# Performance work log

Hardware: AMD Instinct MI355X
Metric: run time of the kernel (lower is better)

Reference implementation:

```python
import jax, jax.numpy as jnp
import numpy as np
from math import sqrt

DIM = 1024
RANK = 64
B, T = 4, 4096

def _xavier(key, shape):
    fan_in, fan_out = shape[1], shape[0]
    limit = sqrt(6.0 / (fan_in + fan_out))
    return jax.random.uniform(key, shape, jnp.float32, -limit, limit)

def setup_inputs() -> dict:
    key = jax.random.key(0)
    kx, kq, kk, kv = jax.random.split(key, 4)
    return {
        "x": jax.random.normal(kx, (B, T, DIM), jnp.float32),
        "Q": _xavier(kq, (RANK, DIM)),
        "K": _xavier(kk, (RANK, DIM)),
        "VO": _xavier(kv, (DIM, DIM)),
    }

def reference(x, Q, K, VO):
    dim = x.shape[-1]
    # low-rank projections: [b, t, r]
    xq = jnp.einsum('btd,rd->btr', x, Q)
    xk = jnp.einsum('bue,re->bur', x, K)
    scores = jnp.einsum('btr,bur->btu', xq, xk) / sqrt(dim)
    attn = jax.nn.softmax(scores, axis=2)
    # attn @ x @ VO: contract with VO first (cheap [b,u,d]@[d,e]) then attn
    return jnp.einsum('btu,bue->bte', attn, x @ VO)
```

## Files before the change

### kernel.cpp

```cpp
#include <hip/hip_runtime.h>
#include <hip/hip_bf16.h>

#define BATCH 4
#define SEQ   4096
#define DIM   1024
#define RANK  64

typedef __attribute__((ext_vector_type(8))) short short8;
typedef __attribute__((ext_vector_type(4))) short short4v;
typedef __attribute__((ext_vector_type(4))) float f32x4;

#define MFMA16(a,b,c) __builtin_amdgcn_mfma_f32_16x16x32_bf16((a),(b),(c),0,0,0)

#define XQ_OFF 0
#define XK_OFF (BATCH*SEQ*RANK)
#define VT_OFF (2*BATCH*SEQ*RANK)
#define VT_END (VT_OFF + BATCH*DIM*SEQ)
#define P_OFF  ((size_t)VT_END)
#define P_LEN  ((size_t)BATCH*SEQ*SEQ)

__device__ __forceinline__ short f2b(float f) {
    __hip_bfloat16 h = __float2bfloat16(f);
    short s; __builtin_memcpy(&s, &h, sizeof(short));
    return s;
}
__device__ __forceinline__ float b2f(short s) {
    __hip_bfloat16 h; __builtin_memcpy(&h, &s, sizeof(short));
    return __bfloat162float(h);
}
__device__ __forceinline__ short8 cvt8(const float* __restrict__ p) {
    const float4 f0 = *reinterpret_cast<const float4*>(p);
    const float4 f1 = *reinterpret_cast<const float4*>(p + 4);
    short8 r;
    r[0]=f2b(f0.x); r[1]=f2b(f0.y); r[2]=f2b(f0.z); r[3]=f2b(f0.w);
    r[4]=f2b(f1.x); r[5]=f2b(f1.y); r[6]=f2b(f1.z); r[7]=f2b(f1.w);
    return r;
}
__device__ __forceinline__ void gld16(const short* g, short* l) {
    __builtin_amdgcn_global_load_lds(
        (const __attribute__((address_space(1))) void*)g,
        (__attribute__((address_space(3))) void*)l, 16, 0, 0);
}

__global__ __launch_bounds__(256) void lr_cvt(const float* __restrict__ x,
                                              const float* __restrict__ VO,
                                              const float* __restrict__ Qw,
                                              const float* __restrict__ Kw,
                                              short* __restrict__ xb,
                                              short* __restrict__ VOt,
                                              short* __restrict__ Wb)
{
    const int bid = blockIdx.x, tid = threadIdx.x;
    if (bid < 8192) {
        const size_t base = ((size_t)bid*256 + tid)*8;
        *reinterpret_cast<short8*>(xb + base) = cvt8(x + base);
    } else if (bid < 8448) {
        __shared__ short tr[64*68];
        const int bb = bid - 8192;
        const int dt = bb >> 4, et = bb & 15;
        const int d0 = dt*64, e0 = et*64;
        const int ein = tid & 63, din = tid >> 6;
        #pragma unroll
        for (int j = 0; j < 16; ++j) {
            const int dl = din + j*4;
            tr[ein*68 + dl] = f2b(VO[(size_t)(d0 + dl)*DIM + e0 + ein]);
        }
        __syncthreads();
        const int or_ = tid >> 4, oc = (tid & 15)*4;
        #pragma unroll
        for (int j = 0; j < 4; ++j) {
            const int el = or_ + j*16;
            short4v v;
            v[0]=tr[el*68+oc]; v[1]=tr[el*68+oc+1];
            v[2]=tr[el*68+oc+2]; v[3]=tr[el*68+oc+3];
            *reinterpret_cast<short4v*>(VOt + (size_t)(e0+el)*DIM + d0 + oc) = v;
        }
    } else {
        const int gid = (bid - 8448)*256 + tid;
        const int row = gid >> 7, c8 = (gid & 127)*8;
        const float* src = (row < 64 ? Qw + (size_t)row*DIM
                                     : Kw + (size_t)(row-64)*DIM) + c8;
        *reinterpret_cast<short8*>(Wb + (size_t)row*DIM + c8) = cvt8(src);
    }
}

__global__ __launch_bounds__(256, 4) void lr_proj2(const short* __restrict__ xb,
                                                   const short* __restrict__ Wb,
                                                   short* __restrict__ ws)
{
    __shared__ __align__(16) short As[128*64];
    __shared__ __align__(16) short Bs[128*64];
    const int t0 = blockIdx.x*128;
    const int tid = threadIdx.x, lane = tid & 63, w = tid >> 6;
    const int l15 = lane & 15, g = lane >> 4;
    const int wr = w >> 1, wc = w & 1;
    const short* Ab = xb + (size_t)t0*DIM;
    const short* Bb = Wb;
    const int srow = lane >> 3;
    const int skc  = ((lane & 7) ^ srow)*8;
    const int rx = l15 & 7;

    f32x4 acc[4][4] = {};
    #pragma unroll
    for (int j = 0; j < 4; ++j) {
        const int ch = 4*w + j, row = ch*8 + srow;
        gld16(Ab + (size_t)row*DIM + skc, &As[ch*512]);
        gld16(Bb + (size_t)row*DIM + skc, &Bs[ch*512]);
    }
    for (int kt = 0; kt < 16; ++kt) {
        __syncthreads();
        #pragma unroll
        for (int ks = 0; ks < 2; ++ks) {
            short8 af[4], bfr[4];
            #pragma unroll
            for (int mr = 0; mr < 4; ++mr)
                af[mr] = *reinterpret_cast<const short8*>(
                    &As[(wr*64 + mr*16 + l15)*64 + ((ks*4 + g) ^ rx)*8]);
            #pragma unroll
            for (int ct = 0; ct < 4; ++ct)
                bfr[ct] = *reinterpret_cast<const short8*>(
                    &Bs[(wc*64 + ct*16 + l15)*64 + ((ks*4 + g) ^ rx)*8]);
            #pragma unroll
            for (int mr = 0; mr < 4; ++mr)
                #pragma unroll
                for (int ct = 0; ct < 4; ++ct)
                    acc[mr][ct] = MFMA16(af[mr], bfr[ct], acc[mr][ct]);
        }
        if (kt < 15) {
            __syncthreads();
            const int k0 = (kt + 1)*64;
            #pragma unroll
            for (int j = 0; j < 4; ++j) {
                const int ch = 4*w + j, row = ch*8 + srow;
                gld16(Ab + (size_t)row*DIM + k0 + skc, &As[ch*512]);
                gld16(Bb + (size_t)row*DIM + k0 + skc, &Bs[ch*512]);
            }
        }
    }
    short* xqp = ws + XQ_OFF;
    short* xkp = ws + XK_OFF;
    #pragma unroll
    for (int mr = 0; mr < 4; ++mr)
        #pragma unroll
        for (int rr = 0; rr < 4; ++rr) {
            const int t = t0 + wr*64 + mr*16 + g*4 + rr;
            #pragma unroll
            for (int ct = 0; ct < 4; ++ct) {
                const int r = wc*64 + ct*16 + l15;
                const short v = f2b(acc[mr][ct][rr]);
                if (r < RANK) xqp[(size_t)t*RANK + r] = v;
                else          xkp[(size_t)t*RANK + r - RANK] = v;
            }
        }
}

__global__ __launch_bounds__(256, 4) void lr_vgemm2(const short* __restrict__ VOt,
                                                    const short* __restrict__ xb,
                                                    short* __restrict__ vT)
{
    __shared__ __align__(16) short As[128*64];
    __shared__ __align__(16) short Bs[128*64];
    const int i = blockIdx.x;
    const int etile = i & 7, j = i >> 3;
    const int ut = j & 31, b = j >> 5;
    const int e0 = etile*128, u0 = ut*128;
    const int tid = threadIdx.x, lane = tid & 63, w = tid >> 6;
    const int l15 = lane & 15, g = lane >> 4;
    const int wr = w >> 1, wc = w & 1;
    const short* Ab = VOt + (size_t)e0*DIM;
    const short* Bb = xb + ((size_t)(b*SEQ) + u0)*DIM;
    const int srow = lane >> 3;
    const int skc  = ((lane & 7) ^ srow)*8;
    const int rx = l15 & 7;

    f32x4 acc[4][4] = {};
    #pragma unroll
    for (int jj = 0; jj < 4; ++jj) {
        const int ch = 4*w + jj, row = ch*8 + srow;
        gld16(Ab + (size_t)row*DIM + skc, &As[ch*512]);
        gld16(Bb + (size_t)row*DIM + skc, &Bs[ch*512]);
    }
    for (int kt = 0; kt < 16; ++kt) {
        __syncthreads();
        #pragma unroll
        for (int ks = 0; ks < 2; ++ks) {
            short8 af[4], bfr[4];
            #pragma unroll
            for (int mr = 0; mr < 4; ++mr)
                af[mr] = *reinterpret_cast<const short8*>(
                    &As[(wr*64 + mr*16 + l15)*64 + ((ks*4 + g) ^ rx)*8]);
            #pragma unroll
            for (int ct = 0; ct < 4; ++ct)
                bfr[ct] = *reinterpret_cast<const short8*>(
                    &Bs[(wc*64 + ct*16 + l15)*64 + ((ks*4 + g) ^ rx)*8]);
            #pragma unroll
            for (int mr = 0; mr < 4; ++mr)
                #pragma unroll
                for (int ct = 0; ct < 4; ++ct)
                    acc[mr][ct] = MFMA16(af[mr], bfr[ct], acc[mr][ct]);
        }
        if (kt < 15) {
            __syncthreads();
            const int k0 = (kt + 1)*64;
            #pragma unroll
            for (int jj = 0; jj < 4; ++jj) {
                const int ch = 4*w + jj, row = ch*8 + srow;
                gld16(Ab + (size_t)row*DIM + k0 + skc, &As[ch*512]);
                gld16(Bb + (size_t)row*DIM + k0 + skc, &Bs[ch*512]);
            }
        }
    }
    #pragma unroll
    for (int mr = 0; mr < 4; ++mr)
        #pragma unroll
        for (int rr = 0; rr < 4; ++rr) {
            const int e = e0 + wr*64 + mr*16 + g*4 + rr;
            short* orow = vT + ((size_t)(b*DIM) + e)*SEQ + u0 + wc*64;
            #pragma unroll
            for (int ct = 0; ct < 4; ++ct)
                orow[ct*16 + l15] = f2b(acc[mr][ct][rr]);
        }
}

__global__ __launch_bounds__(256, 4) void lr_pexp(const short* __restrict__ ws,
                                                  short* __restrict__ P,
                                                  float* __restrict__ ps)
{
    __shared__ __align__(16) short ptile[128*136];
    __shared__ float sred[4][128];
    const int i = blockIdx.x;
    const int qt = i >> 5, ut = i & 31;
    const int b = qt >> 5;
    const int tid = threadIdx.x, lane = tid & 63, w = tid >> 6;
    const int l15 = lane & 15, g = lane >> 4;
    const float cl = 0.045084220f;
    const int q0 = qt*128;

    const short* xqb = ws + XQ_OFF + (size_t)q0*RANK;
    const short* xkb = ws + XK_OFF + ((size_t)(b*SEQ) + ut*128)*RANK;

    f32x4 acc[2][8] = {};
    #pragma unroll
    for (int ks = 0; ks < 2; ++ks) {
        short8 ak[2], bq[8];
        #pragma unroll
        for (int mr = 0; mr < 2; ++mr)
            ak[mr] = *reinterpret_cast<const short8*>(
                xkb + (size_t)(32*w + mr*16 + l15)*RANK + ks*32 + g*8);
        #pragma unroll
        for (int ct = 0; ct < 8; ++ct)
            bq[ct] = *reinterpret_cast<const short8*>(
                xqb + (size_t)(ct*16 + l15)*RANK + ks*32 + g*8);
        #pragma unroll
        for (int mr = 0; mr < 2; ++mr)
            #pragma unroll
            for (int ct = 0; ct < 8; ++ct)
                acc[mr][ct] = MFMA16(ak[mr], bq[ct], acc[mr][ct]);
    }
    float s[8] = {0.f,0.f,0.f,0.f,0.f,0.f,0.f,0.f};
    #pragma unroll
    for (int mr = 0; mr < 2; ++mr)
        #pragma unroll
        for (int ct = 0; ct < 8; ++ct) {
            short4v pk;
            #pragma unroll
            for (int r = 0; r < 4; ++r) {
                const short pb = f2b(__builtin_amdgcn_exp2f(acc[mr][ct][r]*cl));
                pk[r] = pb;
                s[ct] += b2f(pb);
            }
            *reinterpret_cast<short4v*>(
                &ptile[(ct*16 + l15)*136 + 32*w + mr*16 + g*4]) = pk;
        }
    #pragma unroll
    for (int ct = 0; ct < 8; ++ct) {
        s[ct] += __shfl_xor(s[ct], 16);
        s[ct] += __shfl_xor(s[ct], 32);
    }
    if (g == 0) {
        #pragma unroll
        for (int ct = 0; ct < 8; ++ct) sred[w][ct*16 + l15] = s[ct];
    }
    __syncthreads();
    #pragma unroll
    for (int j = 0; j < 8; ++j) {
        const int id = tid + 256*j;
        const int row = id >> 4, seg = id & 15;
        const uint4 v = *reinterpret_cast<const uint4*>(&ptile[row*136 + seg*8]);
        *reinterpret_cast<uint4*>(
            P + (size_t)(q0 + row)*SEQ + ut*128 + seg*8) = v;
    }
    if (tid < 128)
        ps[(size_t)(q0 + tid)*32 + ut] =
            sred[0][tid] + sred[1][tid] + sred[2][tid] + sred[3][tid];
}

__global__ __launch_bounds__(256) void lr_psum(const float* __restrict__ ps,
                                               float* __restrict__ linv)
{
    const int gq = blockIdx.x*256 + threadIdx.x;
    const float* p = ps + (size_t)gq*32;
    float s = 0.f;
    #pragma unroll
    for (int j = 0; j < 32; ++j) s += p[j];
    linv[gq] = 1.0f / s;
}

__global__ __launch_bounds__(512, 2) void lr_pv8(const short* __restrict__ P,
                                                 const short* __restrict__ vT,
                                                 const float* __restrict__ linv,
                                                 float* __restrict__ out)
{
    extern __shared__ __align__(16) short lds[];
    short* As = lds;
    short* Bs = lds + 32768;
    const int bid = blockIdx.x;
    const int qt = (bid & 7)*8 + (bid >> 5);
    const int nt = (bid >> 3) & 3;
    const int q0 = qt*256, d0 = nt*256, b = qt >> 4;
    const int tid = threadIdx.x, lane = tid & 63, w = tid >> 6;
    const int wr = w >> 2, wc = w & 3;
    const int l15 = lane & 15, g = lane >> 4;
    const int rx = l15 & 7;

    const short* Ab = P + (size_t)q0*SEQ;
    const short* Bb = vT + ((size_t)(b*DIM) + d0)*SEQ;

    int aA0[2], aA1[2], aB0[2], aB1[2];
    int dA0[2], dA1[2], dB0[2], dB1[2];
    #pragma unroll
    for (int j = 0; j < 2; ++j) {
        const int s = tid + 512*j;
        const int cl = s >> 6, v = s & 63;
        const int vr = v >> 3, vk = ((v & 7) ^ vr)*8;
        const int cA0 = (cl < 8) ? cl : cl + 8;
        const int cA1 = cA0 + 8;
        const int cB0 = ((cl >> 2) << 3) + (cl & 3);
        const int cB1 = cB0 + 4;
        aA0[j] = (cA0*8 + vr)*SEQ + vk;  dA0[j] = cA0*512 + v*8;
        aA1[j] = (cA1*8 + vr)*SEQ + vk;  dA1[j] = cA1*512 + v*8;
        aB0[j] = (cB0*8 + vr)*SEQ + vk;  dB0[j] = cB0*512 + v*8;
        aB1[j] = (cB1*8 + vr)*SEQ + vk;  dB1[j] = cB1*512 + v*8;
    }

    f32x4 acc[8][4] = {};
    short8 af[4][2], bf[4][2];

    #pragma unroll
    for (int j = 0; j < 2; ++j) gld16(Ab + aA0[j], &As[dA0[j]]);
    #pragma unroll
    for (int j = 0; j < 2; ++j) gld16(Bb + aB0[j], &Bs[dB0[j]]);
    #pragma unroll
    for (int j = 0; j < 2; ++j) gld16(Bb + aB1[j], &Bs[dB1[j]]);
    #pragma unroll
    for (int j = 0; j < 2; ++j) gld16(Ab + aA1[j], &As[dA1[j]]);
    asm volatile("s_waitcnt vmcnt(4)" ::: "memory");
    __builtin_amdgcn_s_barrier();
    __builtin_amdgcn_sched_barrier(0);

    for (int kt = 0; kt < 63; ++kt) {
        const int buf  = (kt & 1) ? 16384 : 0;
        const int nbuf = 16384 - buf;
        const int kn = (kt + 1)*64;
        const int arow = buf + (wr*128 + l15)*64;
        const int brow = buf + (wc*64 + l15)*64;
        #pragma unroll
        for (int mf = 0; mf < 4; ++mf)
            #pragma unroll
            for (int ks = 0; ks < 2; ++ks)
                af[mf][ks] = *reinterpret_cast<const short8*>(
                    &As[arow + mf*1024 + ((ks*4 + g) ^ rx)*8]);
        #pragma unroll
        for (int nf = 0; nf < 2; ++nf)
            #pragma unroll
            for (int ks = 0; ks < 2; ++ks)
                bf[nf][ks] = *reinterpret_cast<const short8*>(
                    &Bs[brow + nf*1024 + ((ks*4 + g) ^ rx)*8]);
        #pragma unroll
        for (int j = 0; j < 2; ++j) gld16(Ab + aA0[j] + kn, &As[nbuf + dA0[j]]);
        __builtin_amdgcn_s_barrier();
        asm volatile("s_waitcnt lgkmcnt(0)" ::: "memory");
        __builtin_amdgcn_sched_barrier(0);
        __builtin_amdgcn_s_setprio(1);
        #pragma unroll
        for (int mf = 0; mf < 4; ++mf)
            #pragma unroll
            for (int nf = 0; nf < 2; ++nf)
                #pragma unroll
                for (int ks = 0; ks < 2; ++ks)
                    acc[mf][nf] = MFMA16(af[mf][ks], bf[nf][ks], acc[mf][nf]);
        __builtin_amdgcn_s_setprio(0);
        asm volatile("s_waitcnt vmcnt(4)" ::: "memory");
        __builtin_amdgcn_s_barrier();
        __builtin_amdgcn_sched_barrier(0);
        #pragma unroll
        for (int nf = 2; nf < 4; ++nf)
            #pragma unroll
            for (int ks = 0; ks < 2; ++ks)
                bf[nf][ks] = *reinterpret_cast<const short8*>(
                    &Bs[brow + nf*1024 + ((ks*4 + g) ^ rx)*8]);
        #pragma unroll
        for (int j = 0; j < 2; ++j) gld16(Bb + aB0[j] + kn, &Bs[nbuf + dB0[j]]);
        __builtin_amdgcn_s_barrier();
        asm volatile("s_waitcnt lgkmcnt(0)" ::: "memory");
        __builtin_amdgcn_sched_barrier(0);
        __builtin_amdgcn_s_setprio(1);
        #pragma unroll
        for (int mf = 0; mf < 4; ++mf)
            #pragma unroll
            for (int nf = 2; nf < 4; ++nf)
                #pragma unroll
                for (int ks = 0; ks < 2; ++ks)
                    acc[mf][nf] = MFMA16(af[mf][ks], bf[nf][ks], acc[mf][nf]);
        __builtin_amdgcn_s_setprio(0);
        asm volatile("s_waitcnt vmcnt(4)" ::: "memory");
        __builtin_amdgcn_s_barrier();
        __builtin_amdgcn_sched_barrier(0);
        #pragma unroll
        for (int mf = 0; mf < 4; ++mf)
            #pragma unroll
            for (int ks = 0; ks < 2; ++ks)
                af[mf][ks] = *reinterpret_cast<const short8*>(
                    &As[arow + 4096 + mf*1024 + ((ks*4 + g) ^ rx)*8]);
        #pragma unroll
        for (int j = 0; j < 2; ++j) gld16(Bb + aB1[j] + kn, &Bs[nbuf + dB1[j]]);
        __builtin_amdgcn_s_barrier();
        asm volatile("s_waitcnt lgkmcnt(0)" ::: "memory");
        __builtin_amdgcn_sched_barrier(0);
        __builtin_amdgcn_s_setprio(1);
        #pragma unroll
        for (int mf = 0; mf < 4; ++mf)
            #pragma unroll
            for (int nf = 0; nf < 2; ++nf)
                #pragma unroll
                for (int ks = 0; ks < 2; ++ks)
                    acc[mf+4][nf] = MFMA16(af[mf][ks], bf[nf][ks], acc[mf+4][nf]);
        __builtin_amdgcn_s_setprio(0);
        __builtin_amdgcn_s_barrier();
        __builtin_amdgcn_sched_barrier(0);
        #pragma unroll
        for (int j = 0; j < 2; ++j) gld16(Ab + aA1[j] + kn, &As[nbuf + dA1[j]]);
        __builtin_amdgcn_s_setprio(1);
        #pragma unroll
        for (int mf = 0; mf < 4; ++mf)
            #pragma unroll
            for (int nf = 2; nf < 4; ++nf)
                #pragma unroll
                for (int ks = 0; ks < 2; ++ks)
                    acc[mf+4][nf] = MFMA16(af[mf][ks], bf[nf][ks], acc[mf+4][nf]);
        __builtin_amdgcn_s_setprio(0);
        asm volatile("s_waitcnt vmcnt(4)" ::: "memory");
        __builtin_amdgcn_s_barrier();
        __builtin_amdgcn_sched_barrier(0);
    }
    asm volatile("s_waitcnt vmcnt(0)" ::: "memory");
    __builtin_amdgcn_s_barrier();
    __builtin_amdgcn_sched_barrier(0);
    {
        const int arow = 16384 + (wr*128 + l15)*64;
        const int brow = 16384 + (wc*64 + l15)*64;
        #pragma unroll
        for (int mf = 0; mf < 4; ++mf)
            #pragma unroll
            for (int ks = 0; ks < 2; ++ks)
                af[mf][ks] = *reinterpret_cast<const short8*>(
                    &As[arow + mf*1024 + ((ks*4 + g) ^ rx)*8]);
        #pragma unroll
        for (int nf = 0; nf < 4; ++nf)
            #pragma unroll
            for (int ks = 0; ks < 2; ++ks)
                bf[nf][ks] = *reinterpret_cast<const short8*>(
                    &Bs[brow + nf*1024 + ((ks*4 + g) ^ rx)*8]);
        #pragma unroll
        for (int mf = 0; mf < 4; ++mf)
            #pragma unroll
            for (int nf = 0; nf < 4; ++nf)
                #pragma unroll
                for (int ks = 0; ks < 2; ++ks)
                    acc[mf][nf] = MFMA16(af[mf][ks], bf[nf][ks], acc[mf][nf]);
        #pragma unroll
        for (int mf = 0; mf < 4; ++mf)
            #pragma unroll
            for (int ks = 0; ks < 2; ++ks)
                af[mf][ks] = *reinterpret_cast<const short8*>(
                    &As[arow + 4096 + mf*1024 + ((ks*4 + g) ^ rx)*8]);
        #pragma unroll
        for (int mf = 0; mf < 4; ++mf)
            #pragma unroll
            for (int nf = 0; nf < 4; ++nf)
                #pragma unroll
                for (int ks = 0; ks < 2; ++ks)
                    acc[mf+4][nf] = MFMA16(af[mf][ks], bf[nf][ks], acc[mf+4][nf]);
    }
    #pragma unroll
    for (int mf = 0; mf < 8; ++mf)
        #pragma unroll
        for (int rr = 0; rr < 4; ++rr) {
            const int q = q0 + wr*128 + mf*16 + g*4 + rr;
            const float sc = linv[q];
            float* rp = out + (size_t)q*DIM + d0 + wc*64;
            #pragma unroll
            for (int nf = 0; nf < 4; ++nf)
                rp[nf*16 + l15] = acc[mf][nf][rr]*sc;
        }
}

__global__ __launch_bounds__(256, 4) void lr_pv(const short* __restrict__ P,
                                                const short* __restrict__ vT,
                                                const float* __restrict__ linv,
                                                float* __restrict__ out)
{
    __shared__ __align__(16) short As[128*64];
    __shared__ __align__(16) short Bs[128*64];
    const int i = blockIdx.x;
    const int qlo = i & 7, j = i >> 3;
    const int nt = j & 7, qhi = j >> 3;
    const int qt = qhi*8 + qlo;
    const int q0 = qt*128, d0 = nt*128, b = qt >> 5;
    const int tid = threadIdx.x, lane = tid & 63, w = tid >> 6;
    const int l15 = lane & 15, g = lane >> 4;
    const int wr = w >> 1, wc = w & 1;

    const short* Ab = P + (size_t)q0*SEQ;
    const short* Bb = vT + ((size_t)(b*DIM) + d0)*SEQ;
    const int srow = lane >> 3;
    const int skc  = ((lane & 7) ^ srow)*8;
    const int rx = l15 & 7;

    f32x4 acc[4][4] = {};
    #pragma unroll
    for (int jj = 0; jj < 4; ++jj) {
        const int ch = 4*w + jj, row = ch*8 + srow;
        gld16(Ab + (size_t)row*SEQ + skc, &As[ch*512]);
        gld16(Bb + (size_t)row*SEQ + skc, &Bs[ch*512]);
    }
    for (int kt = 0; kt < 64; ++kt) {
        __syncthreads();
        #pragma unroll
        for (int ks = 0; ks < 2; ++ks) {
            short8 af[4], bfr[4];
            #pragma unroll
            for (int mr = 0; mr < 4; ++mr)
                af[mr] = *reinterpret_cast<const short8*>(
                    &As[(wr*64 + mr*16 + l15)*64 + ((ks*4 + g) ^ rx)*8]);
            #pragma unroll
            for (int ct = 0; ct < 4; ++ct)
                bfr[ct] = *reinterpret_cast<const short8*>(
                    &Bs[(wc*64 + ct*16 + l15)*64 + ((ks*4 + g) ^ rx)*8]);
            #pragma unroll
            for (int mr = 0; mr < 4; ++mr)
                #pragma unroll
                for (int ct = 0; ct < 4; ++ct)
                    acc[mr][ct] = MFMA16(af[mr], bfr[ct], acc[mr][ct]);
        }
        if (kt < 63) {
            __syncthreads();
            const int k0 = (kt + 1)*64;
            #pragma unroll
            for (int jj = 0; jj < 4; ++jj) {
                const int ch = 4*w + jj, row = ch*8 + srow;
                gld16(Ab + (size_t)row*SEQ + k0 + skc, &As[ch*512]);
                gld16(Bb + (size_t)row*SEQ + k0 + skc, &Bs[ch*512]);
            }
        }
    }
    #pragma unroll
    for (int mr = 0; mr < 4; ++mr)
        #pragma unroll
        for (int rr = 0; rr < 4; ++rr) {
            const int q = q0 + wr*64 + mr*16 + g*4 + rr;
            const float sc = linv[q];
            float* rp = out + (size_t)q*DIM + d0 + wc*64;
            #pragma unroll
            for (int ct = 0; ct < 4; ++ct)
                rp[ct*16 + l15] = acc[mr][ct][rr]*sc;
        }
}

__global__ __launch_bounds__(256) void lr_proj(const float* __restrict__ x,
                                               const float* __restrict__ Qw,
                                               const float* __restrict__ Kw,
                                               short* __restrict__ ws)
{
    __shared__ __align__(16) short ldsB[64*40];
    const int i = blockIdx.x;
    const int ttile = i & 63, b = i >> 6;
    const int tid = threadIdx.x, lane = tid & 63, w = tid >> 6;
    const int l15 = lane & 15, g = lane >> 4;
    const int t0 = ttile * 64;

    f32x4 acc[2][4] = {};
    for (int e0 = 0; e0 < DIM; e0 += 32) {
        const int tr = tid >> 2, seg = tid & 3;
        const float* px = x + (size_t)(b*SEQ + t0 + tr)*DIM + e0 + seg*8;
        const float4 f0 = *reinterpret_cast<const float4*>(px);
        const float4 f1 = *reinterpret_cast<const float4*>(px + 4);
        __syncthreads();
        {
            short* d = &ldsB[tr*40 + seg*8];
            d[0]=f2b(f0.x); d[1]=f2b(f0.y); d[2]=f2b(f0.z); d[3]=f2b(f0.w);
            d[4]=f2b(f1.x); d[5]=f2b(f1.y); d[6]=f2b(f1.z); d[7]=f2b(f1.w);
        }
        __syncthreads();
        #pragma unroll
        for (int mr = 0; mr < 2; ++mr) {
            const int r = 32*w + mr*16 + l15;
            const float* wp = (r < RANK ? Qw + (size_t)r*DIM
                                        : Kw + (size_t)(r - RANK)*DIM) + e0 + g*8;
            const short8 a = cvt8(wp);
            #pragma unroll
            for (int ct = 0; ct < 4; ++ct) {
                const short8 bb = *reinterpret_cast<const short8*>(
                    &ldsB[(ct*16 + l15)*40 + g*8]);
                acc[mr][ct] = MFMA16(a, bb, acc[mr][ct]);
            }
        }
    }
    short* xqp = ws + XQ_OFF;
    short* xkp = ws + XK_OFF;
    #pragma unroll
    for (int mr = 0; mr < 2; ++mr) {
        const int rb = 32*w + mr*16 + g*4;
        short* base = (rb < RANK) ? (xqp + rb) : (xkp + (rb - RANK));
        #pragma unroll
        for (int ct = 0; ct < 4; ++ct) {
            const int t = t0 + ct*16 + l15;
            short4v pk;
            pk[0]=f2b(acc[mr][ct][0]); pk[1]=f2b(acc[mr][ct][1]);
            pk[2]=f2b(acc[mr][ct][2]); pk[3]=f2b(acc[mr][ct][3]);
            *reinterpret_cast<short4v*>(base + (size_t)(b*SEQ + t)*RANK) = pk;
        }
    }
}

__global__ __launch_bounds__(256) void lr_vgemm(const float* __restrict__ x,
                                                const float* __restrict__ VO,
                                                short* __restrict__ ws)
{
    short* vT = ws + VT_OFF;
    __shared__ __align__(16) short ldsA[128*40];
    __shared__ __align__(16) short ldsB[128*40];
    const int i = blockIdx.x;
    const int dtile = i & 7, utile = (i >> 3) & 31, b = i >> 8;
    const int d0 = dtile*128, u0 = utile*128;
    const int tid = threadIdx.x, lane = tid & 63, w = tid >> 6;
    const int l15 = lane & 15, g = lane >> 4;
    const int wr = w >> 1, wc = w & 1;

    f32x4 acc[4][4] = {};
    for (int e0 = 0; e0 < DIM; e0 += 32) {
        const int dcol = tid & 127, erg = (tid >> 7)*16;
        float va[16];
        #pragma unroll
        for (int j = 0; j < 16; ++j)
            va[j] = VO[(size_t)(e0 + erg + j)*DIM + d0 + dcol];
        const int ur = tid >> 1, esg = (tid & 1)*16;
        const float* pb = x + (size_t)(b*SEQ + u0 + ur)*DIM + e0 + esg;
        float4 vb0 = reinterpret_cast<const float4*>(pb)[0];
        float4 vb1 = reinterpret_cast<const float4*>(pb)[1];
        float4 vb2 = reinterpret_cast<const float4*>(pb)[2];
        float4 vb3 = reinterpret_cast<const float4*>(pb)[3];
        __syncthreads();
        #pragma unroll
        for (int j = 0; j < 16; ++j) ldsA[dcol*40 + erg + j] = f2b(va[j]);
        {
            short* d = &ldsB[ur*40 + esg];
            d[0]=f2b(vb0.x); d[1]=f2b(vb0.y); d[2]=f2b(vb0.z); d[3]=f2b(vb0.w);
            d[4]=f2b(vb1.x); d[5]=f2b(vb1.y); d[6]=f2b(vb1.z); d[7]=f2b(vb1.w);
            d[8]=f2b(vb2.x); d[9]=f2b(vb2.y); d[10]=f2b(vb2.z); d[11]=f2b(vb2.w);
            d[12]=f2b(vb3.x); d[13]=f2b(vb3.y); d[14]=f2b(vb3.z); d[15]=f2b(vb3.w);
        }
        __syncthreads();
        short8 af[4], bfr[4];
        #pragma unroll
        for (int mr = 0; mr < 4; ++mr)
            af[mr] = *reinterpret_cast<const short8*>(
                &ldsA[(wr*64 + mr*16 + l15)*40 + g*8]);
        #pragma unroll
        for (int ct = 0; ct < 4; ++ct)
            bfr[ct] = *reinterpret_cast<const short8*>(
                &ldsB[(wc*64 + ct*16 + l15)*40 + g*8]);
        #pragma unroll
        for (int mr = 0; mr < 4; ++mr)
            #pragma unroll
            for (int ct = 0; ct < 4; ++ct)
                acc[mr][ct] = MFMA16(af[mr], bfr[ct], acc[mr][ct]);
    }
    #pragma unroll
    for (int mr = 0; mr < 4; ++mr)
        #pragma unroll
        for (int rr = 0; rr < 4; ++rr) {
            const int d = d0 + wr*64 + mr*16 + g*4 + rr;
            short* orow = vT + (size_t)(b*DIM + d)*SEQ + u0 + wc*64;
            #pragma unroll
            for (int ct = 0; ct < 4; ++ct)
                orow[ct*16 + l15] = f2b(acc[mr][ct][rr]);
        }
}

__global__ __launch_bounds__(256) void lr_stats(const short* __restrict__ ws,
                                                float* __restrict__ pm,
                                                float* __restrict__ pl)
{
    const short* xq = ws + XQ_OFF;
    const short* xk = ws + XK_OFF;
    const int i = blockIdx.x;
    const int us = i & 3, qtile = (i >> 2) & 63, b = i >> 8;
    const int tid = threadIdx.x, lane = tid & 63, w = tid >> 6;
    const int l15 = lane & 15, g = lane >> 4;
    const float cl = 0.045084220f;

    short8 qb0, qb1;
    {
        const short* p = xq + (size_t)(b*SEQ + qtile*64 + 16*w + l15)*RANK + g*8;
        qb0 = *reinterpret_cast<const short8*>(p);
        qb1 = *reinterpret_cast<const short8*>(p + 32);
    }
    const short* kb = xk + (size_t)b*SEQ*RANK;

    float m = -3.0e38f, l = 0.f;
    for (int it = 0; it < 16; ++it) {
        const int ub = us*1024 + it*64;
        f32x4 S[4];
        #pragma unroll
        for (int t = 0; t < 4; ++t) {
            const short* kp = kb + (size_t)(ub + 16*t + l15)*RANK + g*8;
            const short8 a0 = *reinterpret_cast<const short8*>(kp);
            const short8 a1 = *reinterpret_cast<const short8*>(kp + 32);
            f32x4 z = {};
            z = MFMA16(a0, qb0, z);
            z = MFMA16(a1, qb1, z);
            S[t] = z;
        }
        float mt = S[0][0];
        #pragma unroll
        for (int t = 0; t < 4; ++t)
            #pragma unroll
            for (int r = 0; r < 4; ++r) mt = fmaxf(mt, S[t][r]);
        const float mn = fmaxf(m, mt);
        l *= __builtin_amdgcn_exp2f((m - mn)*cl);
        const float mc = mn*cl;
        #pragma unroll
        for (int t = 0; t < 4; ++t)
            #pragma unroll
            for (int r = 0; r < 4; ++r)
                l += __builtin_amdgcn_exp2f(__builtin_fmaf(S[t][r], cl, -mc));
        m = mn;
    }
    #pragma unroll
    for (int mask = 16; mask <= 32; mask <<= 1) {
        const float mo = __shfl_xor(m, mask), lo = __shfl_xor(l, mask);
        const float mn = fmaxf(m, mo);
        l = l*__builtin_amdgcn_exp2f((m - mn)*cl)
          + lo*__builtin_amdgcn_exp2f((mo - mn)*cl);
        m = mn;
    }
    if (g == 0) {
        const int idx = (b*SEQ + qtile*64 + 16*w + l15)*4 + us;
        pm[idx] = m; pl[idx] = l;
    }
}

__global__ __launch_bounds__(256, 4) void lr_flash(const short* __restrict__ ws,
                                                   const float* __restrict__ pm,
                                                   const float* __restrict__ pl,
                                                   float* __restrict__ out)
{
    const short* xq = ws + XQ_OFF;
    const short* xk = ws + XK_OFF;
    const short* vT = ws + VT_OFF;
    __shared__ __align__(16) short vlds[128*64];
    __shared__ __align__(16) short plds[32*64];
    const int i = blockIdx.x;
    const int xcd = i & 7, slot = i >> 3;
    const int combo = xcd + 8*(slot >> 6);
    const int qtile = slot & 63;
    const int b = combo >> 2, dch = combo & 3;
    const int tid = threadIdx.x, lane = tid & 63, w = tid >> 6;
    const int l15 = lane & 15, g = lane >> 4;
    const float cl = 0.045084220f;

    float mC;
    {
        const int base = (b*SEQ + qtile*64 + 16*w + l15)*4;
        const float m0 = pm[base+0], m1 = pm[base+1];
        const float m2 = pm[base+2], m3 = pm[base+3];
        const float mm = fmaxf(fmaxf(m0, m1), fmaxf(m2, m3));
        const float l = pl[base+0]*__builtin_amdgcn_exp2f((m0-mm)*cl)
                      + pl[base+1]*__builtin_amdgcn_exp2f((m1-mm)*cl)
                      + pl[base+2]*__builtin_amdgcn_exp2f((m2-mm)*cl)
                      + pl[base+3]*__builtin_amdgcn_exp2f((m3-mm)*cl);
        mC = -(mm*cl + __builtin_amdgcn_logf(l));
    }
    short8 qb0, qb1;
    {
        const short* p = xq + (size_t)(b*SEQ + qtile*64 + 16*w + l15)*RANK + g*8;
        qb0 = *reinterpret_cast<const short8*>(p);
        qb1 = *reinterpret_cast<const short8*>(p + 32);
    }
    const short* vbase = vT + ((size_t)b*DIM + dch*256)*SEQ;
    const short* kr = xk + (size_t)b*SEQ*RANK + l15*RANK + g*8;
    const int r7 = l15 >> 1;
    const int st_dst = (tid >> 3)*64 + (((tid & 7) ^ ((tid >> 3) & 7))*8);
    const int st_src = (tid >> 2)*SEQ + (tid & 3)*8;
    const int a_base = r7*64 + ((((l15 & 1)*4 + g) ^ r7)*8);
    const int b_base = (32*w + r7)*64 + ((((l15 & 1)*4 + g) ^ r7)*8);
    const int chv = (l15 & 1)*4 + (g >> 1);
    const int pw0 = (8*w + r7)*64 + ((chv ^ r7)*8)       + (g & 1)*4;
    const int pw1 = (8*w + r7)*64 + (((chv + 2) ^ r7)*8) + (g & 1)*4;

    uint4 sreg[4];
    #pragma unroll
    for (int c = 0; c < 4; ++c)
        sreg[c] = *reinterpret_cast<const uint4*>(vbase + st_src + (size_t)c*64*SEQ);
    #pragma unroll
    for (int c = 0; c < 4; ++c)
        *reinterpret_cast<uint4*>(&vlds[st_dst + 2048*c]) = sreg[c];

    f32x4 O[16] = {};
    for (int ub = 0; ub < SEQ; ub += 32) {
        const bool more = (ub + 32 < SEQ);
        if (more) {
            #pragma unroll
            for (int c = 0; c < 4; ++c)
                sreg[c] = *reinterpret_cast<const uint4*>(
                    vbase + st_src + ub + 32 + (size_t)c*64*SEQ);
        }
        #pragma unroll
        for (int t = 0; t < 2; ++t) {
            const short* kp = kr + (size_t)(ub + 16*t)*RANK;
            const short8 a0 = *reinterpret_cast<const short8*>(kp);
            const short8 a1 = *reinterpret_cast<const short8*>(kp + 32);
            f32x4 z = {};
            z = MFMA16(a0, qb0, z);
            z = MFMA16(a1, qb1, z);
            short4v pk;
            #pragma unroll
            for (int r = 0; r < 4; ++r)
                pk[r] = f2b(__builtin_amdgcn_exp2f(__builtin_fmaf(z[r], cl, mC)));
            *reinterpret_cast<short4v*>(&plds[t ? pw1 : pw0]) = pk;
        }
        __syncthreads();
        short8 pa[4];
        #pragma unroll
        for (int qt = 0; qt < 4; ++qt)
            pa[qt] = *reinterpret_cast<const short8*>(&plds[a_base + qt*512]);
        #pragma unroll
        for (int dt = 0; dt < 4; ++dt) {
            const short8 vf = *reinterpret_cast<const short8*>(&vlds[b_base + dt*512]);
            #pragma unroll
            for (int qt = 0; qt < 4; ++qt)
                O[qt*4 + dt] = MFMA16(pa[qt], vf, O[qt*4 + dt]);
        }
        __syncthreads();
        if (more) {
            #pragma unroll
            for (int c = 0; c < 4; ++c)
                *reinterpret_cast<uint4*>(&vlds[st_dst + 2048*c]) = sreg[c];
        }
    }
    #pragma unroll
    for (int qt = 0; qt < 4; ++qt)
        #pragma unroll
        for (int rr = 0; rr < 4; ++rr) {
            const int q = qtile*64 + qt*16 + g*4 + rr;
            float* rowp = out + (size_t)(b*SEQ + q)*DIM + dch*256 + 64*w;
            #pragma unroll
            for (int dt = 0; dt < 4; ++dt)
                rowp[dt*16 + l15] = O[qt*4 + dt][rr];
        }
}

extern "C" void kernel_launch(void* const* d_in, const int* in_sizes, int n_in,
                              void* d_out, int out_size, void* d_ws, size_t ws_size,
                              hipStream_t stream) {
    const float* x  = (const float*)d_in[0];
    const float* Q  = (const float*)d_in[1];
    const float* K  = (const float*)d_in[2];
    const float* VO = (const float*)d_in[3];
    float* out = (float*)d_out;
    short* ws = (short*)d_ws;

    const size_t need = (P_OFF + P_LEN)*2 + (size_t)(BATCH*SEQ)*(32 + 1)*4;
    if (ws_size >= need) {
        short* Pb  = ws + P_OFF;
        short* xb  = Pb;
        short* VOt = Pb + (size_t)BATCH*SEQ*DIM;
        short* Wb  = VOt + (size_t)DIM*DIM;
        float* ps  = (float*)(ws + P_OFF + P_LEN);
        float* linv = ps + (size_t)BATCH*SEQ*32;
        lr_cvt   <<<dim3(8512), dim3(256), 0, stream>>>(x, VO, Q, K, xb, VOt, Wb);
        lr_proj2 <<<dim3(128),  dim3(256), 0, stream>>>(xb, Wb, ws);
        lr_vgemm2<<<dim3(1024), dim3(256), 0, stream>>>(VOt, xb, ws + VT_OFF);
        lr_pexp  <<<dim3(4096), dim3(256), 0, stream>>>(ws, Pb, ps);
        lr_psum  <<<dim3(64),   dim3(256), 0, stream>>>(ps, linv);
        const hipError_t e = hipFuncSetAttribute(
            reinterpret_cast<const void*>(lr_pv8),
            hipFuncAttributeMaxDynamicSharedMemorySize, 131072);
        if (e == hipSuccess)
            lr_pv8<<<dim3(256), dim3(512), 131072, stream>>>(Pb, ws + VT_OFF, linv, out);
        else
            lr_pv <<<dim3(1024), dim3(256), 0, stream>>>(Pb, ws + VT_OFF, linv, out);
    } else {
        float* pm = (float*)(ws + VT_END);
        float* pl = pm + BATCH*SEQ*4;
        lr_proj <<<dim3(256),  dim3(256), 0, stream>>>(x, Q, K, ws);
        lr_stats<<<dim3(1024), dim3(256), 0, stream>>>(ws, pm, pl);
        lr_vgemm<<<dim3(1024), dim3(256), 0, stream>>>(x, VO, ws);
        lr_flash<<<dim3(1024), dim3(256), 0, stream>>>(ws, pm, pl, out);
    }
}
```

Baseline: 246.4 us.

## Use 256x256-tile 512-thread VO GEMM and fold row-sum reduction into PV kernel

Adds lr_vg8, a 256x256-tile VO-projection GEMM with 512 threads, 128 KB dynamic LDS, and a pipeline of interleaved global-to-LDS prefetch and MFMA phases, modeled on the existing lr_pv8. It replaces the 128x128 lr_vgemm2 to raise data reuse per block. The separate lr_psum launch is also removed: lr_pv8 now sums the 32 partial row sums for its 256 rows into LDS at kernel start, saving one launch. The cost is a small serial reduction prologue in every PV block and the lower occupancy of the larger GEMM tiles.

```diff
diff --git a/kernel.cpp b/kernel.cpp
--- a/kernel.cpp
+++ b/kernel.cpp
@@ -154,6 +154,205 @@
         }
 }
 
+__global__ __launch_bounds__(512, 2) void lr_vg8(const short* __restrict__ VOt,
+                                                 const short* __restrict__ xb,
+                                                 short* __restrict__ vT)
+{
+    extern __shared__ __align__(16) short lds[];
+    short* As = lds;
+    short* Bs = lds + 32768;
+    const int bid = blockIdx.x;
+    const int xcd = bid & 7, jb = bid >> 3;
+    const int et = xcd >> 1;
+    const int bu = (xcd & 1)*32 + jb;
+    const int b = bu >> 4, ut = bu & 15;
+    const int e0 = et*256, u0 = ut*256;
+    const int tid = threadIdx.x, lane = tid & 63, w = tid >> 6;
+    const int wr = w >> 2, wc = w & 3;
+    const int l15 = lane & 15, g = lane >> 4;
+    const int rx = l15 & 7;
+
+    const short* Ab = VOt + (size_t)e0*DIM;
+    const short* Bb = xb + ((size_t)(b*SEQ) + u0)*DIM;
+
+    int aA0[2], aA1[2], aB0[2], aB1[2];
+    int dA0[2], dA1[2], dB0[2], dB1[2];
+    #pragma unroll
+    for (int j = 0; j < 2; ++j) {
+        const int s = tid + 512*j;
+        const int cl = s >> 6, v = s & 63;
+        const int vr = v >> 3, vk = ((v & 7) ^ vr)*8;
+        const int cA0 = (cl < 8) ? cl : cl + 8;
+        const int cA1 = cA0 + 8;
+        const int cB0 = ((cl >> 2) << 3) + (cl & 3);
+        const int cB1 = cB0 + 4;
+        aA0[j] = (cA0*8 + vr)*DIM + vk;  dA0[j] = cA0*512 + v*8;
+        aA1[j] = (cA1*8 + vr)*DIM + vk;  dA1[j] = cA1*512 + v*8;
+        aB0[j] = (cB0*8 + vr)*DIM + vk;  dB0[j] = cB0*512 + v*8;
+        aB1[j] = (cB1*8 + vr)*DIM + vk;  dB1[j] = cB1*512 + v*8;
+    }
+
+    f32x4 acc[8][4] = {};
+    short8 af[4][2], bf[4][2];
+
+    #pragma unroll
+    for (int j = 0; j < 2; ++j) gld16(Ab + aA0[j], &As[dA0[j]]);
+    #pragma unroll
+    for (int j = 0; j < 2; ++j) gld16(Bb + aB0[j], &Bs[dB0[j]]);
+    #pragma unroll
+    for (int j = 0; j < 2; ++j) gld16(Bb + aB1[j], &Bs[dB1[j]]);
+    #pragma unroll
+    for (int j = 0; j < 2; ++j) gld16(Ab + aA1[j], &As[dA1[j]]);
+    asm volatile("s_waitcnt vmcnt(4)" ::: "memory");
+    __builtin_amdgcn_s_barrier();
+    __builtin_amdgcn_sched_barrier(0);
+
+    for (int kt = 0; kt < 15; ++kt) {
+        const int buf  = (kt & 1) ? 16384 : 0;
+        const int nbuf = 16384 - buf;
+        const int kn = (kt + 1)*64;
+        const int arow = buf + (wr*128 + l15)*64;
+        const int brow = buf + (wc*64 + l15)*64;
+        #pragma unroll
+        for (int mf = 0; mf < 4; ++mf)
+            #pragma unroll
+            for (int ks = 0; ks < 2; ++ks)
+                af[mf][ks] = *reinterpret_cast<const short8*>(
+                    &As[arow + mf*1024 + ((ks*4 + g) ^ rx)*8]);
+        #pragma unroll
+        for (int nf = 0; nf < 2; ++nf)
+            #pragma unroll
+            for (int ks = 0; ks < 2; ++ks)
+                bf[nf][ks] = *reinterpret_cast<const short8*>(
+                    &Bs[brow + nf*1024 + ((ks*4 + g) ^ rx)*8]);
+        #pragma unroll
+        for (int j = 0; j < 2; ++j) gld16(Ab + aA0[j] + kn, &As[nbuf + dA0[j]]);
+        __builtin_amdgcn_s_barrier();
+        asm volatile("s_waitcnt lgkmcnt(0)" ::: "memory");
+        __builtin_amdgcn_sched_barrier(0);
+        __builtin_amdgcn_s_setprio(1);
+        #pragma unroll
+        for (int mf = 0; mf < 4; ++mf)
+            #pragma unroll
+            for (int nf = 0; nf < 2; ++nf)
+                #pragma unroll
+                for (int ks = 0; ks < 2; ++ks)
+                    acc[mf][nf] = MFMA16(af[mf][ks], bf[nf][ks], acc[mf][nf]);
+        __builtin_amdgcn_s_setprio(0);
+        asm volatile("s_waitcnt vmcnt(4)" ::: "memory");
+        __builtin_amdgcn_s_barrier();
+        __builtin_amdgcn_sched_barrier(0);
+        #pragma unroll
+        for (int nf = 2; nf < 4; ++nf)
+            #pragma unroll
+            for (int ks = 0; ks < 2; ++ks)
+                bf[nf][ks] = *reinterpret_cast<const short8*>(
+                    &Bs[brow + nf*1024 + ((ks*4 + g) ^ rx)*8]);
+        #pragma unroll
+        for (int j = 0; j < 2; ++j) gld16(Bb + aB0[j] + kn, &Bs[nbuf + dB0[j]]);
+        __builtin_amdgcn_s_barrier();
+        asm volatile("s_waitcnt lgkmcnt(0)" ::: "memory");
+        __builtin_amdgcn_sched_barrier(0);
+        __builtin_amdgcn_s_setprio(1);
+        #pragma unroll
+        for (int mf = 0; mf < 4; ++mf)
+            #pragma unroll
+            for (int nf = 2; nf < 4; ++nf)
+                #pragma unroll
+                for (int ks = 0; ks < 2; ++ks)
+                    acc[mf][nf] = MFMA16(af[mf][ks], bf[nf][ks], acc[mf][nf]);
+        __builtin_amdgcn_s_setprio(0);
+        asm volatile("s_waitcnt vmcnt(4)" ::: "memory");
+        __builtin_amdgcn_s_barrier();
+        __builtin_amdgcn_sched_barrier(0);
+        #pragma unroll
+        for (int mf = 0; mf < 4; ++mf)
+            #pragma unroll
+            for (int ks = 0; ks < 2; ++ks)
+                af[mf][ks] = *reinterpret_cast<const short8*>(
+                    &As[arow + 4096 + mf*1024 + ((ks*4 + g) ^ rx)*8]);
+        #pragma unroll
+        for (int j = 0; j < 2; ++j) gld16(Bb + aB1[j] + kn, &Bs[nbuf + dB1[j]]);
+        __builtin_amdgcn_s_barrier();
+        asm volatile("s_waitcnt lgkmcnt(0)" ::: "memory");
+        __builtin_amdgcn_sched_barrier(0);
+        __builtin_amdgcn_s_setprio(1);
+        #pragma unroll
+        for (int mf = 0; mf < 4; ++mf)
+            #pragma unroll
+            for (int nf = 0; nf < 2; ++nf)
+                #pragma unroll
+                for (int ks = 0; ks < 2; ++ks)
+                    acc[mf+4][nf] = MFMA16(af[mf][ks], bf[nf][ks], acc[mf+4][nf]);
+        __builtin_amdgcn_s_setprio(0);
+        __builtin_amdgcn_s_barrier();
+        __builtin_amdgcn_sched_barrier(0);
+        #pragma unroll
+        for (int j = 0; j < 2; ++j) gld16(Ab + aA1[j] + kn, &As[nbuf + dA1[j]]);
+        __builtin_amdgcn_s_setprio(1);
+        #pragma unroll
+        for (int mf = 0; mf < 4; ++mf)
+            #pragma unroll
+            for (int nf = 2; nf < 4; ++nf)
+                #pragma unroll
+                for (int ks = 0; ks < 2; ++ks)
+                    acc[mf+4][nf] = MFMA16(af[mf][ks], bf[nf][ks], acc[mf+4][nf]);
+        __builtin_amdgcn_s_setprio(0);
+        asm volatile("s_waitcnt vmcnt(4)" ::: "memory");
+        __builtin_amdgcn_s_barrier();
+        __builtin_amdgcn_sched_barrier(0);
+    }
+    asm volatile("s_waitcnt vmcnt(0)" ::: "memory");
+    __builtin_amdgcn_s_barrier();
+    __builtin_amdgcn_sched_barrier(0);
+    {
+        const int arow = 16384 + (wr*128 + l15)*64;
+        const int brow = 16384 + (wc*64 + l15)*64;
+        #pragma unroll
+        for (int mf = 0; mf < 4; ++mf)
+            #pragma unroll
+            for (int ks = 0; ks < 2; ++ks)
+                af[mf][ks] = *reinterpret_cast<const short8*>(
+                    &As[arow + mf*1024 + ((ks*4 + g) ^ rx)*8]);
+        #pragma unroll
+        for (int nf = 0; nf < 4; ++nf)
+            #pragma unroll
+            for (int ks = 0; ks < 2; ++ks)
+                bf[nf][ks] = *reinterpret_cast<const short8*>(
+                    &Bs[brow + nf*1024 + ((ks*4 + g) ^ rx)*8]);
+        #pragma unroll
+        for (int mf = 0; mf < 4; ++mf)
+            #pragma unroll
+            for (int nf = 0; nf < 4; ++nf)
+                #pragma unroll
+                for (int ks = 0; ks < 2; ++ks)
+                    acc[mf][nf] = MFMA16(af[mf][ks], bf[nf][ks], acc[mf][nf]);
+        #pragma unroll
+        for (int mf = 0; mf < 4; ++mf)
+            #pragma unroll
+            for (int ks = 0; ks < 2; ++ks)
+                af[mf][ks] = *reinterpret_cast<const short8*>(
+                    &As[arow + 4096 + mf*1024 + ((ks*4 + g) ^ rx)*8]);
+        #pragma unroll
+        for (int mf = 0; mf < 4; ++mf)
+            #pragma unroll
+            for (int nf = 0; nf < 4; ++nf)
+                #pragma unroll
+                for (int ks = 0; ks < 2; ++ks)
+                    acc[mf+4][nf] = MFMA16(af[mf][ks], bf[nf][ks], acc[mf+4][nf]);
+    }
+    #pragma unroll
+    for (int mf = 0; mf < 8; ++mf)
+        #pragma unroll
+        for (int rr = 0; rr < 4; ++rr) {
+            const int e = e0 + wr*128 + mf*16 + g*4 + rr;
+            short* orow = vT + ((size_t)(b*DIM) + e)*SEQ + u0 + wc*64;
+            #pragma unroll
+            for (int nf = 0; nf < 4; ++nf)
+                orow[nf*16 + l15] = f2b(acc[mf][nf][rr]);
+        }
+}
+
 __global__ __launch_bounds__(256, 4) void lr_vgemm2(const short* __restrict__ VOt,
                                                     const short* __restrict__ xb,
                                                     short* __restrict__ vT)
@@ -308,10 +507,11 @@
 
 __global__ __launch_bounds__(512, 2) void lr_pv8(const short* __restrict__ P,
                                                  const short* __restrict__ vT,
-                                                 const float* __restrict__ linv,
+                                                 const float* __restrict__ ps,
                                                  float* __restrict__ out)
 {
     extern __shared__ __align__(16) short lds[];
+    __shared__ float linv_lds[256];
     short* As = lds;
     short* Bs = lds + 32768;
     const int bid = blockIdx.x;
@@ -322,6 +522,16 @@
     const int wr = w >> 2, wc = w & 3;
     const int l15 = lane & 15, g = lane >> 4;
     const int rx = l15 & 7;
+
+    if (tid < 256) {
+        const float* pp = ps + (size_t)(q0 + tid)*32;
+        float s = 0.f;
+        #pragma unroll
+        for (int jj = 0; jj < 32; ++jj) s += pp[jj];
+        linv_lds[tid] = 1.0f / s;
+    }
+    asm volatile("s_waitcnt vmcnt(0)" ::: "memory");
+    __builtin_amdgcn_sched_barrier(0);
 
     const short* Ab = P + (size_t)q0*SEQ;
     const short* Bb = vT + ((size_t)(b*DIM) + d0)*SEQ;
@@ -496,9 +706,9 @@
     for (int mf = 0; mf < 8; ++mf)
         #pragma unroll
         for (int rr = 0; rr < 4; ++rr) {
-            const int q = q0 + wr*128 + mf*16 + g*4 + rr;
-            const float sc = linv[q];
-            float* rp = out + (size_t)q*DIM + d0 + wc*64;
+            const int ql = wr*128 + mf*16 + g*4 + rr;
+            const float sc = linv_lds[ql];
+            float* rp = out + (size_t)(q0 + ql)*DIM + d0 + wc*64;
             #pragma unroll
             for (int nf = 0; nf < 4; ++nf)
                 rp[nf*16 + l15] = acc[mf][nf][rr]*sc;
@@ -889,18 +1099,25 @@
         short* Wb  = VOt + (size_t)DIM*DIM;
         float* ps  = (float*)(ws + P_OFF + P_LEN);
         float* linv = ps + (size_t)BATCH*SEQ*32;
+        const hipError_t e1 = hipFuncSetAttribute(
+            reinterpret_cast<const void*>(lr_pv8),
+            hipFuncAttributeMaxDynamicSharedMemorySize, 131072);
+        const hipError_t e2 = hipFuncSetAttribute(
+            reinterpret_cast<const void*>(lr_vg8),
+            hipFuncAttributeMaxDynamicSharedMemorySize, 131072);
         lr_cvt   <<<dim3(8512), dim3(256), 0, stream>>>(x, VO, Q, K, xb, VOt, Wb);
         lr_proj2 <<<dim3(128),  dim3(256), 0, stream>>>(xb, Wb, ws);
-        lr_vgemm2<<<dim3(1024), dim3(256), 0, stream>>>(VOt, xb, ws + VT_OFF);
+        if (e2 == hipSuccess)
+            lr_vg8   <<<dim3(256), dim3(512), 131072, stream>>>(VOt, xb, ws + VT_OFF);
+        else
+            lr_vgemm2<<<dim3(1024), dim3(256), 0, stream>>>(VOt, xb, ws + VT_OFF);
         lr_pexp  <<<dim3(4096), dim3(256), 0, stream>>>(ws, Pb, ps);
-        lr_psum  <<<dim3(64),   dim3(256), 0, stream>>>(ps, linv);
-        const hipError_t e = hipFuncSetAttribute(
-            reinterpret_cast<const void*>(lr_pv8),
-            hipFuncAttributeMaxDynamicSharedMemorySize, 131072);
-        if (e == hipSuccess)
-            lr_pv8<<<dim3(256), dim3(512), 131072, stream>>>(Pb, ws + VT_OFF, linv, out);
-        else
-            lr_pv <<<dim3(1024), dim3(256), 0, stream>>>(Pb, ws + VT_OFF, linv, out);
+        if (e1 == hipSuccess) {
+            lr_pv8<<<dim3(256), dim3(512), 131072, stream>>>(Pb, ws + VT_OFF, ps, out);
+        } else {
+            lr_psum<<<dim3(64), dim3(256), 0, stream>>>(ps, linv);
+            lr_pv  <<<dim3(1024), dim3(256), 0, stream>>>(Pb, ws + VT_OFF, linv, out);
+        }
     } else {
         float* pm = (float*)(ws + VT_END);
         float* pl = pm + BATCH*SEQ*4;
```

New measurement: 235.9 us (median of 2 runs). -4.3%, faster.
